# Optimization experiments

Hardware: AMD Instinct MI355X
Metric: run time of the kernel (lower is better)

Reference implementation:

```python
import jax, jax.numpy as jnp
import numpy as np

N_NODES = 100000
N_EDGES = 1600000
IN_F = 128
OUT_F = 32
HEADS = 4
NEG_SLOPE = 0.2
EPS = 1e-8


def setup_inputs() -> dict:
    key = jax.random.key(0)
    k1, k2, k3, k4 = jax.random.split(key, 4)
    x = jax.random.normal(k1, (N_NODES, IN_F), dtype=jnp.float32)
    # torch Linear weight layout: [out_features*num_heads, in_features]
    # xavier_uniform-like scale
    limW = float(np.sqrt(6.0 / (IN_F + OUT_F * HEADS)))
    W = jax.random.uniform(k2, (OUT_F * HEADS, IN_F), dtype=jnp.float32, minval=-limW, maxval=limW)
    lima = float(np.sqrt(6.0 / (HEADS + 2 * OUT_F)))
    a = jax.random.uniform(k3, (HEADS, 2 * OUT_F), dtype=jnp.float32, minval=-lima, maxval=lima)
    edge_index = jax.random.randint(k4, (2, N_EDGES), 0, N_NODES, dtype=jnp.int64)
    return {"x": x, "W": W, "a": a, "edge_index": edge_index}


def reference(x, W, a, edge_index):
    # x: [N, in], W: [H*F, in], a: [H, 2F], edge_index: [2, E]
    N = x.shape[0]
    H = HEADS
    F = OUT_F
    h = (x @ W.T).reshape(N, H, F)                      # [N, H, F]
    src, dst = edge_index[0], edge_index[1]
    h_src = h[src]                                       # [E, H, F]
    h_dst = h[dst]                                       # [E, H, F]
    # (cat([h_src, h_dst], -1) * a).sum(-1) == h_src@a_src + h_dst@a_dst
    a_src, a_dst = a[:, :F], a[:, F:]
    att = jnp.einsum('ehf,hf->eh', h_src, a_src) + jnp.einsum('ehf,hf->eh', h_dst, a_dst)  # [E, H]
    att = jnp.where(att >= 0, att, NEG_SLOPE * att)      # leaky_relu(0.2)
    att = jnp.exp(att - att.max())                       # global-max stabilization (as in source)
    att_sum = jax.ops.segment_sum(att, dst, num_segments=N)    # [N, H]
    att = att / (att_sum[dst] + EPS)                     # segment softmax
    # dropout is identity in eval mode
    out = jax.ops.segment_sum(att[..., None] * h_src, dst, num_segments=N)  # [N, H, F]
    return out.reshape(N, H * F)                         # concat=True
```

## Files before the change

kernel.cpp:

```cpp
#include <hip/hip_runtime.h>
#include <hip/hip_bf16.h>

#define NEG_SLOPE 0.2f
#define EPSV 1e-8f
#define BCAP 5632

typedef float f32x4 __attribute__((ext_vector_type(4)));
typedef short bf16x8 __attribute__((ext_vector_type(8)));
typedef unsigned short us8 __attribute__((ext_vector_type(8)));

static __device__ __forceinline__ float bf16tof(unsigned short s) {
    union { unsigned u; float f; } c; c.u = ((unsigned)s) << 16; return c.f;
}
static __device__ __forceinline__ unsigned short ftobf16(float f) {
    __hip_bfloat16 b = __float2bfloat16(f);
    return *(unsigned short*)&b;
}
static __device__ __forceinline__ float leaky_exp(float v) {
    v = fmaxf(v, NEG_SLOPE * v);
    return __expf(v);
}

__global__ __launch_bounds__(256, 2) void k_gemm_scatter(
        const float* __restrict__ x, const float* __restrict__ W,
        const float* __restrict__ a, unsigned short* __restrict__ h_bf,
        float* __restrict__ asrc, float* __restrict__ adst,
        const int* __restrict__ ei, int* __restrict__ relcur,
        unsigned* __restrict__ ebuf, int E, int N, int GB, int SB) {
    __shared__ unsigned short xs[128 * 128];
    __shared__ unsigned short ws[128 * 128];
    __shared__ float sa[256];
    int tid = threadIdx.x;
    int bid = blockIdx.x;

    int M = min(GB, SB);
    bool isGemm; int myIdx;
    if (bid < 2 * M) { isGemm = ((bid & 1) == 0); myIdx = bid >> 1; }
    else { isGemm = (GB > SB); myIdx = bid - M; }

    if (!isGemm) {
        int* hist  = (int*)xs;
        int* wcur  = hist + 512;
        int* bslot = wcur + 512;
        int lo = myIdx * 2048;
        int hi = min(E, lo + 2048);
        hist[tid] = 0; hist[tid + 256] = 0;
        wcur[tid] = 0; wcur[tid + 256] = 0;
        __syncthreads();
        int sreg[8], dreg[8];
#pragma unroll
        for (int k = 0; k < 8; k++) {
            int e = lo + tid + 256 * k;
            if (e < hi) {
                sreg[k] = ei[e];
                dreg[k] = ei[E + e];
                atomicAdd(&hist[dreg[k] >> 8], 1);
            }
        }
        __syncthreads();
        int c0 = hist[tid], c1 = hist[tid + 256];
        int r0 = c0 ? atomicAdd(&relcur[tid], c0) : 0;
        int r1 = c1 ? atomicAdd(&relcur[tid + 256], c1) : 0;
        bslot[tid]       = tid * BCAP + r0;
        bslot[tid + 256] = (tid + 256) * BCAP + r1;
        __syncthreads();
#pragma unroll
        for (int k = 0; k < 8; k++) {
            int e = lo + tid + 256 * k;
            if (e < hi) {
                int s = sreg[k];
                int d = dreg[k];
                int b = d >> 8;
                int off = atomicAdd(&wcur[b], 1);
                int slot = bslot[b] + off;
                if (slot < (b + 1) * BCAP)
                    ebuf[slot] = ((unsigned)(d & 255) << 23) | (unsigned)s;
            }
        }
        return;
    }

    int nb = myIdx * 128;
    sa[tid] = a[tid];

#pragma unroll
    for (int it = 0; it < 16; ++it) {
        int f = tid + 256 * it;
        int row = f >> 5;
        int k0 = (f & 31) << 2;
        int sw = row * 128 + (k0 ^ ((row & 7) << 3));
        int n = nb + row; if (n >= N) n = N - 1;
        float4 v = *(const float4*)(x + (size_t)n * 128 + k0);
        ushort4 o;
        o.x = ftobf16(v.x); o.y = ftobf16(v.y);
        o.z = ftobf16(v.z); o.w = ftobf16(v.w);
        *(ushort4*)&xs[sw] = o;
        float4 wv = *(const float4*)(W + (size_t)row * 128 + k0);
        ushort4 ow;
        ow.x = ftobf16(wv.x); ow.y = ftobf16(wv.y);
        ow.z = ftobf16(wv.z); ow.w = ftobf16(wv.w);
        *(ushort4*)&ws[sw] = ow;
    }
    __syncthreads();

    int w  = tid >> 6;
    int l  = tid & 63;
    int lr = l & 15;
    int lg = l >> 4;

    f32x4 acc[2][8];
    {
        f32x4 zz = {0.f, 0.f, 0.f, 0.f};
#pragma unroll
        for (int nt = 0; nt < 2; ++nt)
#pragma unroll
            for (int jt = 0; jt < 8; ++jt)
                acc[nt][jt] = zz;
    }

#pragma unroll
    for (int ks = 0; ks < 4; ++ks) {
        int kofs = ks * 32 + lg * 8;
        bf16x8 xf[2];
#pragma unroll
        for (int nt = 0; nt < 2; ++nt) {
            int row = w * 32 + nt * 16 + lr;
            xf[nt] = *(const bf16x8*)&xs[row * 128 + (kofs ^ ((row & 7) << 3))];
        }
#pragma unroll
        for (int jt = 0; jt < 8; ++jt) {
            int j = jt * 16 + lr;
            bf16x8 wf = *(const bf16x8*)&ws[j * 128 + (kofs ^ ((j & 7) << 3))];
#pragma unroll
            for (int nt = 0; nt < 2; ++nt)
                acc[nt][jt] = __builtin_amdgcn_mfma_f32_16x16x32_bf16(
                    wf, xf[nt], acc[nt][jt], 0, 0, 0);
        }
    }

#pragma unroll
    for (int g = 0; g < 4; ++g) {
        f32x4 as0 = *(const f32x4*)&sa[g * 64 +      lg * 4];
        f32x4 as1 = *(const f32x4*)&sa[g * 64 + 16 + lg * 4];
        f32x4 ad0 = *(const f32x4*)&sa[g * 64 + 32 + lg * 4];
        f32x4 ad1 = *(const f32x4*)&sa[g * 64 + 48 + lg * 4];
#pragma unroll
        for (int nt = 0; nt < 2; ++nt) {
            float ps = 0.f, pd = 0.f;
#pragma unroll
            for (int r = 0; r < 4; ++r) {
                ps += acc[nt][2 * g][r] * as0[r] + acc[nt][2 * g + 1][r] * as1[r];
                pd += acc[nt][2 * g][r] * ad0[r] + acc[nt][2 * g + 1][r] * ad1[r];
            }
            ps += __shfl_xor(ps, 16); pd += __shfl_xor(pd, 16);
            ps += __shfl_xor(ps, 32); pd += __shfl_xor(pd, 32);
            if (lg == 0) {
                int n = nb + w * 32 + nt * 16 + lr;
                if (n < N) {
                    asrc[(size_t)n * 4 + g] = ps;
                    adst[(size_t)n * 4 + g] = pd;
                }
            }
        }
    }

    __syncthreads();
#pragma unroll
    for (int nt = 0; nt < 2; ++nt) {
        int row = w * 32 + nt * 16 + lr;
        int m = (row & 7) << 3;
#pragma unroll
        for (int jt = 0; jt < 8; ++jt) {
            int j0 = jt * 16 + lg * 4;
            ushort4 o;
            o.x = ftobf16(acc[nt][jt][0]);
            o.y = ftobf16(acc[nt][jt][1]);
            o.z = ftobf16(acc[nt][jt][2]);
            o.w = ftobf16(acc[nt][jt][3]);
            *(ushort4*)&xs[row * 128 + (j0 ^ m)] = o;
        }
    }
    __syncthreads();
#pragma unroll
    for (int it = 0; it < 8; ++it) {
        int f = tid + 256 * it;
        int row = f >> 4;
        int c8 = (f & 15) << 3;
        int n = nb + row;
        if (n < N) {
            us8 v = *(const us8*)&xs[row * 128 + (c8 ^ ((row & 7) << 3))];
            *(us8*)(h_bf + (size_t)n * 128 + c8) = v;
        }
    }
}

__global__ __launch_bounds__(512) void k_build(const int* __restrict__ relcur,
        const unsigned* __restrict__ ebuf,
        int* __restrict__ row_ptr, int* __restrict__ csr_src,
        int NBK, int N, int E) {
    __shared__ int smA[512];
    __shared__ int hist[256];
    __shared__ int smB[256];
    int b = blockIdx.x;
    int t = threadIdx.x;

    smA[t] = (t < NBK) ? min(relcur[t], BCAP) : 0;
    __syncthreads();
    for (int off = 1; off < 512; off <<= 1) {
        int u = (t >= off) ? smA[t - off] : 0;
        __syncthreads();
        smA[t] += u;
        __syncthreads();
    }
    int cnt  = min(relcur[b], BCAP);
    int base = smA[b] - cnt;
    if (b == 0 && t == 0) row_ptr[N] = E;

    int d0 = b << 8;
    const unsigned* ep = ebuf + (size_t)b * BCAP;

    if (t < 256) hist[t] = 0;
    __syncthreads();
    unsigned pay[11]; int rnk[11];
#pragma unroll
    for (int k = 0; k < 11; ++k) {
        int i = t + 512 * k;
        if (i < cnt) {
            unsigned p = ep[i];
            pay[k] = p;
            rnk[k] = atomicAdd(&hist[p >> 23], 1);
        } else {
            pay[k] = 0u;
            rnk[k] = -1;
        }
    }
    __syncthreads();

    int s = (t < 256) ? hist[t] : 0;
    if (t < 256) smB[t] = s;
    __syncthreads();
    for (int off = 1; off < 256; off <<= 1) {
        int u = (t >= off && t < 256) ? smB[t - off] : 0;
        __syncthreads();
        if (t < 256) smB[t] += u;
        __syncthreads();
    }
    if (t < 256) {
        int ex = smB[t] - s;
        hist[t] = ex;
        int node = d0 + t;
        if (node < N) row_ptr[node] = base + ex;
    }
    __syncthreads();

#pragma unroll
    for (int k = 0; k < 11; ++k) {
        if (rnk[k] >= 0) {
            unsigned p = pay[k];
            csr_src[base + hist[p >> 23] + rnk[k]] = (int)(p & 0x7FFFFFu);
        }
    }
}

__global__ __launch_bounds__(256) void k_agg(
        const int* __restrict__ row_ptr, const int* __restrict__ csr_src,
        const float* __restrict__ asrc, const float* __restrict__ adst,
        const unsigned short* __restrict__ h_bf,
        float* __restrict__ out, int N) {
    __shared__ int   se[4][2][68];
    __shared__ float sw[4][2][272];
    int tid = threadIdx.x;
    int w  = tid >> 6;
    int l  = tid & 63;
    int gg = l >> 4;
    int m  = l & 15;
    int hh = m >> 2;

    int n = blockIdx.x * 16 + w * 4 + gg;
    bool valid = (n < N);
    int nc = valid ? n : (N - 1);
    int lo  = row_ptr[nc];
    int deg = row_ptr[nc + 1] - lo;
    float4 dv = *(const float4*)(adst + 4 * (size_t)nc);

    int md = deg;
    md = max(md, __shfl_xor(md, 16));
    md = max(md, __shfl_xor(md, 32));
    int nch = (md + 15) >> 4;

    float acc[8] = {};
    float asum = 0.f;
    const unsigned short* hp = h_bf + 8 * m;

#define ACC8(U, WT) do { \
        union { unsigned u; float f; } q; \
        q.u = (U).x << 16;         acc[0] += (WT) * q.f; \
        q.u = (U).x & 0xFFFF0000u; acc[1] += (WT) * q.f; \
        q.u = (U).y << 16;         acc[2] += (WT) * q.f; \
        q.u = (U).y & 0xFFFF0000u; acc[3] += (WT) * q.f; \
        q.u = (U).z << 16;         acc[4] += (WT) * q.f; \
        q.u = (U).z & 0xFFFF0000u; acc[5] += (WT) * q.f; \
        q.u = (U).w << 16;         acc[6] += (WT) * q.f; \
        q.u = (U).w & 0xFFFF0000u; acc[7] += (WT) * q.f; \
    } while (0)

    if (m < deg) {
        int s = csr_src[lo + m];
        se[w][0][17 * gg + m] = s;
        float4 sv = *(const float4*)(asrc + 4 * (size_t)s);
        float4 wv;
        wv.x = leaky_exp(sv.x + dv.x);
        wv.y = leaky_exp(sv.y + dv.y);
        wv.z = leaky_exp(sv.z + dv.z);
        wv.w = leaky_exp(sv.w + dv.w);
        *(float4*)&sw[w][0][68 * gg + 4 * m] = wv;
    }

    for (int c = 0; c < nch; ++c) {
        int cb = c & 1;
        int sN = 0; float4 svN; bool haveN = false;
        {
            int eN = (c + 1) * 16 + m;
            if (c + 1 < nch && eN < deg) {
                sN = csr_src[lo + eN];
                svN = *(const float4*)(asrc + 4 * (size_t)sN);
                haveN = true;
            }
        }
        __builtin_amdgcn_wave_barrier();
        int base16 = c * 16;
        int cnt = min(deg - base16, 16);
        const int*   sep = &se[w][cb][17 * gg];
        const float* swp = &sw[w][cb][68 * gg];
        int i = 0;
        uint4 u0, u1;
        if (cnt >= 2) {
            u0 = *(const uint4*)(hp + (size_t)sep[0] * 128);
            u1 = *(const uint4*)(hp + (size_t)sep[1] * 128);
        }
        for (; i + 4 <= cnt; i += 2) {
            uint4 t0 = *(const uint4*)(hp + (size_t)sep[i + 2] * 128);
            uint4 t1 = *(const uint4*)(hp + (size_t)sep[i + 3] * 128);
            float w0 = swp[4 * i + hh];
            float w1 = swp[4 * i + 4 + hh];
            ACC8(u0, w0);
            ACC8(u1, w1);
            asum += w0 + w1;
            u0 = t0; u1 = t1;
        }
        if (i + 2 <= cnt) {
            float w0 = swp[4 * i + hh];
            float w1 = swp[4 * i + 4 + hh];
            ACC8(u0, w0);
            ACC8(u1, w1);
            asum += w0 + w1;
            i += 2;
        }
        for (; i < cnt; ++i) {
            int s0 = sep[i];
            float w0 = swp[4 * i + hh];
            uint4 uu = *(const uint4*)(hp + (size_t)s0 * 128);
            ACC8(uu, w0);
            asum += w0;
        }
        if (haveN) {
            se[w][cb ^ 1][17 * gg + m] = sN;
            float4 wv;
            wv.x = leaky_exp(svN.x + dv.x);
            wv.y = leaky_exp(svN.y + dv.y);
            wv.z = leaky_exp(svN.z + dv.z);
            wv.w = leaky_exp(svN.w + dv.w);
            *(float4*)&sw[w][cb ^ 1][68 * gg + 4 * m] = wv;
        }
        __builtin_amdgcn_wave_barrier();
    }
#undef ACC8

    if (valid) {
        float inv = 1.f / (asum + EPSV);
        float4 o0, o1;
        o0.x = acc[0] * inv; o0.y = acc[1] * inv;
        o0.z = acc[2] * inv; o0.w = acc[3] * inv;
        o1.x = acc[4] * inv; o1.y = acc[5] * inv;
        o1.z = acc[6] * inv; o1.w = acc[7] * inv;
        *(float4*)(out + (size_t)n * 128 + 8 * m) = o0;
        *(float4*)(out + (size_t)n * 128 + 8 * m + 4) = o1;
    }
}

extern "C" void kernel_launch(void* const* d_in, const int* in_sizes, int n_in,
                              void* d_out, int out_size, void* d_ws, size_t ws_size,
                              hipStream_t stream) {
    const float* x = (const float*)d_in[0];
    const float* W = (const float*)d_in[1];
    const float* a = (const float*)d_in[2];
    const int* ei = (const int*)d_in[3];
    float* out = (float*)d_out;

    int N = in_sizes[0] / 128;
    int E = in_sizes[3] / 2;
    int NBK = (N + 255) >> 8;

    char* wsb = (char*)d_ws;
    size_t off = 0;
    auto alloc = [&](size_t bytes) -> void* {
        void* p = wsb + off;
        off += (bytes + 255) / 256 * 256;
        return p;
    };
    unsigned short* h_bf = (unsigned short*)alloc((size_t)N * 128 * 2);
    float* asrc = (float*)alloc((size_t)N * 4 * 4);
    float* adst = (float*)alloc((size_t)N * 4 * 4);
    int* row_ptr = (int*)alloc((size_t)(N + 1) * 4);
    int* relcur = (int*)alloc(512 * 4);
    unsigned* ebuf = (unsigned*)alloc((size_t)NBK * BCAP * 4);
    int* csr_src = (int*)alloc((size_t)E * 4);

    hipMemsetAsync(relcur, 0, 512 * 4, stream);

    int GB = (N + 127) / 128;
    int SB = (E + 2047) / 2048;
    k_gemm_scatter<<<GB + SB, 256, 0, stream>>>(x, W, a, h_bf, asrc, adst,
                                                ei, relcur, ebuf, E, N, GB, SB);
    k_build<<<NBK, 512, 0, stream>>>(relcur, ebuf, row_ptr, csr_src, NBK, N, E);
    k_agg<<<(N + 15) / 16, 256, 0, stream>>>(row_ptr, csr_src, asrc, adst, h_bf, out, N);
}
```

Baseline: 212.1 us.

## Fuse CSR build into aggregation kernel with per-bucket LDS adjacency

Merges the bucket-sort build kernel and the aggregation kernel into one kernel. Each block sorts its 128-destination bucket into an LDS CSR and then aggregates those nodes directly, which removes the global row_ptr/csr_src arrays, their write and re-read traffic, the global prefix scan, and one launch. Buckets shrink from 256 to 128 nodes with a smaller capacity, and scatter blocks each handle 4096 edges. The cost is fewer, larger aggregation blocks (782 blocks of 512 threads) with heavy LDS use, which may limit occupancy and load balance, and a tighter bucket capacity that could overflow on skewed graphs.

```diff
diff --git a/kernel.cpp b/kernel.cpp
--- a/kernel.cpp
+++ b/kernel.cpp
@@ -3,15 +3,12 @@
 
 #define NEG_SLOPE 0.2f
 #define EPSV 1e-8f
-#define BCAP 5632
+#define BCAP 3072
 
 typedef float f32x4 __attribute__((ext_vector_type(4)));
 typedef short bf16x8 __attribute__((ext_vector_type(8)));
 typedef unsigned short us8 __attribute__((ext_vector_type(8)));
 
-static __device__ __forceinline__ float bf16tof(unsigned short s) {
-    union { unsigned u; float f; } c; c.u = ((unsigned)s) << 16; return c.f;
-}
 static __device__ __forceinline__ unsigned short ftobf16(float f) {
     __hip_bfloat16 b = __float2bfloat16(f);
     return *(unsigned short*)&b;
@@ -40,41 +37,46 @@
 
     if (!isGemm) {
         int* hist  = (int*)xs;
-        int* wcur  = hist + 512;
-        int* bslot = wcur + 512;
-        int lo = myIdx * 2048;
-        int hi = min(E, lo + 2048);
-        hist[tid] = 0; hist[tid + 256] = 0;
-        wcur[tid] = 0; wcur[tid + 256] = 0;
+        int* wcur  = hist + 1024;
+        int* bslot = wcur + 1024;
+        int lo = myIdx * 4096;
+        int hi = min(E, lo + 4096);
+#pragma unroll
+        for (int j = 0; j < 4; ++j) {
+            hist[tid + 256 * j] = 0;
+            wcur[tid + 256 * j] = 0;
+        }
         __syncthreads();
-        int sreg[8], dreg[8];
-#pragma unroll
-        for (int k = 0; k < 8; k++) {
+        int sreg[16], dreg[16];
+#pragma unroll
+        for (int k = 0; k < 16; k++) {
             int e = lo + tid + 256 * k;
             if (e < hi) {
                 sreg[k] = ei[e];
                 dreg[k] = ei[E + e];
-                atomicAdd(&hist[dreg[k] >> 8], 1);
+                atomicAdd(&hist[dreg[k] >> 7], 1);
             }
         }
         __syncthreads();
-        int c0 = hist[tid], c1 = hist[tid + 256];
-        int r0 = c0 ? atomicAdd(&relcur[tid], c0) : 0;
-        int r1 = c1 ? atomicAdd(&relcur[tid + 256], c1) : 0;
-        bslot[tid]       = tid * BCAP + r0;
-        bslot[tid + 256] = (tid + 256) * BCAP + r1;
+#pragma unroll
+        for (int j = 0; j < 4; ++j) {
+            int bb = tid + 256 * j;
+            int c = hist[bb];
+            int r = c ? atomicAdd(&relcur[bb], c) : 0;
+            bslot[bb] = bb * BCAP + r;
+        }
         __syncthreads();
 #pragma unroll
-        for (int k = 0; k < 8; k++) {
+        for (int k = 0; k < 16; k++) {
             int e = lo + tid + 256 * k;
             if (e < hi) {
                 int s = sreg[k];
                 int d = dreg[k];
-                int b = d >> 8;
+                int b = d >> 7;
                 int off = atomicAdd(&wcur[b], 1);
                 int slot = bslot[b] + off;
                 if (slot < (b + 1) * BCAP)
-                    ebuf[slot] = ((unsigned)(d & 255) << 23) | (unsigned)s;
+                    ebuf[slot] = ((unsigned)(d & 127) << 23) | (unsigned)s;
             }
         }
         return;
@@ -194,36 +196,27 @@
     }
 }
 
-__global__ __launch_bounds__(512) void k_build(const int* __restrict__ relcur,
-        const unsigned* __restrict__ ebuf,
-        int* __restrict__ row_ptr, int* __restrict__ csr_src,
-        int NBK, int N, int E) {
-    __shared__ int smA[512];
-    __shared__ int hist[256];
-    __shared__ int smB[256];
+__global__ __launch_bounds__(512) void k_bagg(
+        const int* __restrict__ relcur, const unsigned* __restrict__ ebuf,
+        const float* __restrict__ asrc, const float* __restrict__ adst,
+        const unsigned short* __restrict__ h_bf,
+        float* __restrict__ out, int N) {
+    __shared__ int   csr_lds[BCAP];
+    __shared__ int   offx[128];
+    __shared__ int   dg[128];
+    __shared__ int   hist[128];
+    __shared__ int   smB[128];
+    __shared__ float swb[8][2][272];
     int b = blockIdx.x;
     int t = threadIdx.x;
-
-    smA[t] = (t < NBK) ? min(relcur[t], BCAP) : 0;
-    __syncthreads();
-    for (int off = 1; off < 512; off <<= 1) {
-        int u = (t >= off) ? smA[t - off] : 0;
-        __syncthreads();
-        smA[t] += u;
-        __syncthreads();
-    }
-    int cnt  = min(relcur[b], BCAP);
-    int base = smA[b] - cnt;
-    if (b == 0 && t == 0) row_ptr[N] = E;
-
-    int d0 = b << 8;
+    int cnt = min(relcur[b], BCAP);
     const unsigned* ep = ebuf + (size_t)b * BCAP;
 
-    if (t < 256) hist[t] = 0;
-    __syncthreads();
-    unsigned pay[11]; int rnk[11];
-#pragma unroll
-    for (int k = 0; k < 11; ++k) {
+    if (t < 128) hist[t] = 0;
+    __syncthreads();
+    unsigned pay[6]; int rnk[6];
+#pragma unroll
+    for (int k = 0; k < 6; ++k) {
         int i = t + 512 * k;
         if (i < cnt) {
             unsigned p = ep[i];
@@ -236,60 +229,31 @@
     }
     __syncthreads();
 
-    int s = (t < 256) ? hist[t] : 0;
-    if (t < 256) smB[t] = s;
-    __syncthreads();
-    for (int off = 1; off < 256; off <<= 1) {
-        int u = (t >= off && t < 256) ? smB[t - off] : 0;
+    if (t < 128) { int s = hist[t]; dg[t] = s; smB[t] = s; }
+    __syncthreads();
+    for (int off = 1; off < 128; off <<= 1) {
+        int u = (t >= off && t < 128) ? smB[t - off] : 0;
         __syncthreads();
-        if (t < 256) smB[t] += u;
+        if (t < 128) smB[t] += u;
         __syncthreads();
     }
-    if (t < 256) {
-        int ex = smB[t] - s;
-        hist[t] = ex;
-        int node = d0 + t;
-        if (node < N) row_ptr[node] = base + ex;
-    }
-    __syncthreads();
-
-#pragma unroll
-    for (int k = 0; k < 11; ++k) {
+    if (t < 128) offx[t] = smB[t] - dg[t];
+    __syncthreads();
+
+#pragma unroll
+    for (int k = 0; k < 6; ++k) {
         if (rnk[k] >= 0) {
             unsigned p = pay[k];
-            csr_src[base + hist[p >> 23] + rnk[k]] = (int)(p & 0x7FFFFFu);
-        }
-    }
-}
-
-__global__ __launch_bounds__(256) void k_agg(
-        const int* __restrict__ row_ptr, const int* __restrict__ csr_src,
-        const float* __restrict__ asrc, const float* __restrict__ adst,
-        const unsigned short* __restrict__ h_bf,
-        float* __restrict__ out, int N) {
-    __shared__ int   se[4][2][68];
-    __shared__ float sw[4][2][272];
-    int tid = threadIdx.x;
-    int w  = tid >> 6;
-    int l  = tid & 63;
+            csr_lds[offx[p >> 23] + rnk[k]] = (int)(p & 0x7FFFFFu);
+        }
+    }
+    __syncthreads();
+
+    int w  = t >> 6;
+    int l  = t & 63;
     int gg = l >> 4;
     int m  = l & 15;
     int hh = m >> 2;
-
-    int n = blockIdx.x * 16 + w * 4 + gg;
-    bool valid = (n < N);
-    int nc = valid ? n : (N - 1);
-    int lo  = row_ptr[nc];
-    int deg = row_ptr[nc + 1] - lo;
-    float4 dv = *(const float4*)(adst + 4 * (size_t)nc);
-
-    int md = deg;
-    md = max(md, __shfl_xor(md, 16));
-    md = max(md, __shfl_xor(md, 32));
-    int nch = (md + 15) >> 4;
-
-    float acc[8] = {};
-    float asum = 0.f;
     const unsigned short* hp = h_bf + 8 * m;
 
 #define ACC8(U, WT) do { \
@@ -304,88 +268,104 @@
         q.u = (U).w & 0xFFFF0000u; acc[7] += (WT) * q.f; \
     } while (0)
 
-    if (m < deg) {
-        int s = csr_src[lo + m];
-        se[w][0][17 * gg + m] = s;
-        float4 sv = *(const float4*)(asrc + 4 * (size_t)s);
-        float4 wv;
-        wv.x = leaky_exp(sv.x + dv.x);
-        wv.y = leaky_exp(sv.y + dv.y);
-        wv.z = leaky_exp(sv.z + dv.z);
-        wv.w = leaky_exp(sv.w + dv.w);
-        *(float4*)&sw[w][0][68 * gg + 4 * m] = wv;
-    }
-
-    for (int c = 0; c < nch; ++c) {
-        int cb = c & 1;
-        int sN = 0; float4 svN; bool haveN = false;
-        {
-            int eN = (c + 1) * 16 + m;
-            if (c + 1 < nch && eN < deg) {
-                sN = csr_src[lo + eN];
-                svN = *(const float4*)(asrc + 4 * (size_t)sN);
-                haveN = true;
-            }
+    for (int r = 0; r < 4; ++r) {
+        int nl = r * 32 + w * 4 + gg;
+        int n = (b << 7) + nl;
+        bool valid = (n < N);
+        int nc = valid ? n : (N - 1);
+        int lo  = offx[nl];
+        int deg = dg[nl];
+        float4 dv = *(const float4*)(adst + 4 * (size_t)nc);
+
+        int md = deg;
+        md = max(md, __shfl_xor(md, 16));
+        md = max(md, __shfl_xor(md, 32));
+        int nch = (md + 15) >> 4;
+
+        float acc[8] = {};
+        float asum = 0.f;
+
+        if (m < deg) {
+            int s = csr_lds[lo + m];
+            float4 sv = *(const float4*)(asrc + 4 * (size_t)s);
+            float4 wv;
+            wv.x = leaky_exp(sv.x + dv.x);
+            wv.y = leaky_exp(sv.y + dv.y);
+            wv.z = leaky_exp(sv.z + dv.z);
+            wv.w = leaky_exp(sv.w + dv.w);
+            *(float4*)&swb[w][0][68 * gg + 4 * m] = wv;
         }
         __builtin_amdgcn_wave_barrier();
-        int base16 = c * 16;
-        int cnt = min(deg - base16, 16);
-        const int*   sep = &se[w][cb][17 * gg];
-        const float* swp = &sw[w][cb][68 * gg];
-        int i = 0;
-        uint4 u0, u1;
-        if (cnt >= 2) {
-            u0 = *(const uint4*)(hp + (size_t)sep[0] * 128);
-            u1 = *(const uint4*)(hp + (size_t)sep[1] * 128);
-        }
-        for (; i + 4 <= cnt; i += 2) {
-            uint4 t0 = *(const uint4*)(hp + (size_t)sep[i + 2] * 128);
-            uint4 t1 = *(const uint4*)(hp + (size_t)sep[i + 3] * 128);
-            float w0 = swp[4 * i + hh];
-            float w1 = swp[4 * i + 4 + hh];
-            ACC8(u0, w0);
-            ACC8(u1, w1);
-            asum += w0 + w1;
-            u0 = t0; u1 = t1;
-        }
-        if (i + 2 <= cnt) {
-            float w0 = swp[4 * i + hh];
-            float w1 = swp[4 * i + 4 + hh];
-            ACC8(u0, w0);
-            ACC8(u1, w1);
-            asum += w0 + w1;
-            i += 2;
-        }
-        for (; i < cnt; ++i) {
-            int s0 = sep[i];
-            float w0 = swp[4 * i + hh];
-            uint4 uu = *(const uint4*)(hp + (size_t)s0 * 128);
-            ACC8(uu, w0);
-            asum += w0;
-        }
-        if (haveN) {
-            se[w][cb ^ 1][17 * gg + m] = sN;
-            float4 wv;
-            wv.x = leaky_exp(svN.x + dv.x);
-            wv.y = leaky_exp(svN.y + dv.y);
-            wv.z = leaky_exp(svN.z + dv.z);
-            wv.w = leaky_exp(svN.w + dv.w);
-            *(float4*)&sw[w][cb ^ 1][68 * gg + 4 * m] = wv;
-        }
-        __builtin_amdgcn_wave_barrier();
+
+        for (int c = 0; c < nch; ++c) {
+            int cb = c & 1;
+            int sN = 0; float4 svN; bool haveN = false;
+            {
+                int eN = (c + 1) * 16 + m;
+                if (c + 1 < nch && eN < deg) {
+                    sN = csr_lds[lo + eN];
+                    svN = *(const float4*)(asrc + 4 * (size_t)sN);
+                    haveN = true;
+                }
+            }
+            __builtin_amdgcn_wave_barrier();
+            int base16 = c * 16;
+            int ccnt = min(deg - base16, 16);
+            const int*   idp = &csr_lds[lo + base16];
+            const float* swp = &swb[w][cb][68 * gg];
+            int i = 0;
+            uint4 u0, u1;
+            if (ccnt >= 2) {
+                u0 = *(const uint4*)(hp + (size_t)idp[0] * 128);
+                u1 = *(const uint4*)(hp + (size_t)idp[1] * 128);
+            }
+            for (; i + 4 <= ccnt; i += 2) {
+                uint4 t0 = *(const uint4*)(hp + (size_t)idp[i + 2] * 128);
+                uint4 t1 = *(const uint4*)(hp + (size_t)idp[i + 3] * 128);
+                float w0 = swp[4 * i + hh];
+                float w1 = swp[4 * i + 4 + hh];
+                ACC8(u0, w0);
+                ACC8(u1, w1);
+                asum += w0 + w1;
+                u0 = t0; u1 = t1;
+            }
+            if (i + 2 <= ccnt) {
+                float w0 = swp[4 * i + hh];
+                float w1 = swp[4 * i + 4 + hh];
+                ACC8(u0, w0);
+                ACC8(u1, w1);
+                asum += w0 + w1;
+                i += 2;
+            }
+            for (; i < ccnt; ++i) {
+                float w0 = swp[4 * i + hh];
+                uint4 uu = *(const uint4*)(hp + (size_t)idp[i] * 128);
+                ACC8(uu, w0);
+                asum += w0;
+            }
+            if (haveN) {
+                float4 wv;
+                wv.x = leaky_exp(svN.x + dv.x);
+                wv.y = leaky_exp(svN.y + dv.y);
+                wv.z = leaky_exp(svN.z + dv.z);
+                wv.w = leaky_exp(svN.w + dv.w);
+                *(float4*)&swb[w][cb ^ 1][68 * gg + 4 * m] = wv;
+            }
+            __builtin_amdgcn_wave_barrier();
+        }
+
+        if (valid) {
+            float inv = 1.f / (asum + EPSV);
+            float4 o0, o1;
+            o0.x = acc[0] * inv; o0.y = acc[1] * inv;
+            o0.z = acc[2] * inv; o0.w = acc[3] * inv;
+            o1.x = acc[4] * inv; o1.y = acc[5] * inv;
+            o1.z = acc[6] * inv; o1.w = acc[7] * inv;
+            *(float4*)(out + (size_t)n * 128 + 8 * m) = o0;
+            *(float4*)(out + (size_t)n * 128 + 8 * m + 4) = o1;
+        }
     }
 #undef ACC8
-
-    if (valid) {
-        float inv = 1.f / (asum + EPSV);
-        float4 o0, o1;
-        o0.x = acc[0] * inv; o0.y = acc[1] * inv;
-        o0.z = acc[2] * inv; o0.w = acc[3] * inv;
-        o1.x = acc[4] * inv; o1.y = acc[5] * inv;
-        o1.z = acc[6] * inv; o1.w = acc[7] * inv;
-        *(float4*)(out + (size_t)n * 128 + 8 * m) = o0;
-        *(float4*)(out + (size_t)n * 128 + 8 * m + 4) = o1;
-    }
 }
 
 extern "C" void kernel_launch(void* const* d_in, const int* in_sizes, int n_in,
@@ -399,7 +379,7 @@
 
     int N = in_sizes[0] / 128;
     int E = in_sizes[3] / 2;
-    int NBK = (N + 255) >> 8;
+    int NBK = (N + 127) >> 7;
 
     char* wsb = (char*)d_ws;
     size_t off = 0;
@@ -411,17 +391,14 @@
     unsigned short* h_bf = (unsigned short*)alloc((size_t)N * 128 * 2);
     float* asrc = (float*)alloc((size_t)N * 4 * 4);
     float* adst = (float*)alloc((size_t)N * 4 * 4);
-    int* row_ptr = (int*)alloc((size_t)(N + 1) * 4);
-    int* relcur = (int*)alloc(512 * 4);
+    int* relcur = (int*)alloc(1024 * 4);
     unsigned* ebuf = (unsigned*)alloc((size_t)NBK * BCAP * 4);
-    int* csr_src = (int*)alloc((size_t)E * 4);
-
-    hipMemsetAsync(relcur, 0, 512 * 4, stream);
+
+    hipMemsetAsync(relcur, 0, 1024 * 4, stream);
 
     int GB = (N + 127) / 128;
-    int SB = (E + 2047) / 2048;
+    int SB = (E + 4095) / 4096;
     k_gemm_scatter<<<GB + SB, 256, 0, stream>>>(x, W, a, h_bf, asrc, adst,
                                                 ei, relcur, ebuf, E, N, GB, SB);
-    k_build<<<NBK, 512, 0, stream>>>(relcur, ebuf, row_ptr, csr_src, NBK, N, E);
-    k_agg<<<(N + 15) / 16, 256, 0, stream>>>(row_ptr, csr_src, asrc, adst, h_bf, out, N);
+    k_bagg<<<NBK, 512, 0, stream>>>(relcur, ebuf, asrc, adst, h_bf, out, N);
 }
```

Result: slower. 224.1 us (+5.6%).

## Split aggregation into two feature-half passes with 8 lanes per node

Applied to the files above, without the earlier changes.

The aggregation kernel now runs twice, each pass covering half of the 128 features (two heads), with 8 lanes per node instead of 16 so that 32 nodes are handled per block. Each pass gathers only 128 bytes of h per source row, which shrinks the gather working set per pass and may improve cache hit rates. In exchange, row_ptr, csr_src and the attention scores are read twice, the exp weights are computed twice, and there is an extra kernel launch.

```diff
diff --git a/kernel.cpp b/kernel.cpp
--- a/kernel.cpp
+++ b/kernel.cpp
@@ -9,9 +9,6 @@
 typedef short bf16x8 __attribute__((ext_vector_type(8)));
 typedef unsigned short us8 __attribute__((ext_vector_type(8)));
 
-static __device__ __forceinline__ float bf16tof(unsigned short s) {
-    union { unsigned u; float f; } c; c.u = ((unsigned)s) << 16; return c.f;
-}
 static __device__ __forceinline__ unsigned short ftobf16(float f) {
     __hip_bfloat16 b = __float2bfloat16(f);
     return *(unsigned short*)&b;
@@ -266,31 +263,32 @@
         const int* __restrict__ row_ptr, const int* __restrict__ csr_src,
         const float* __restrict__ asrc, const float* __restrict__ adst,
         const unsigned short* __restrict__ h_bf,
-        float* __restrict__ out, int N) {
-    __shared__ int   se[4][2][68];
-    __shared__ float sw[4][2][272];
+        float* __restrict__ out, int N, int fh) {
+    __shared__ int   se[4][2][8 * 17];
+    __shared__ float sw[4][2][8 * 34];
     int tid = threadIdx.x;
     int w  = tid >> 6;
     int l  = tid & 63;
-    int gg = l >> 4;
-    int m  = l & 15;
+    int gg = l >> 3;
+    int m  = l & 7;
     int hh = m >> 2;
 
-    int n = blockIdx.x * 16 + w * 4 + gg;
+    int n = blockIdx.x * 32 + w * 8 + gg;
     bool valid = (n < N);
     int nc = valid ? n : (N - 1);
     int lo  = row_ptr[nc];
     int deg = row_ptr[nc + 1] - lo;
-    float4 dv = *(const float4*)(adst + 4 * (size_t)nc);
+    float2 dv = *(const float2*)(adst + 4 * (size_t)nc + 2 * fh);
 
     int md = deg;
+    md = max(md, __shfl_xor(md, 8));
     md = max(md, __shfl_xor(md, 16));
     md = max(md, __shfl_xor(md, 32));
     int nch = (md + 15) >> 4;
 
     float acc[8] = {};
     float asum = 0.f;
-    const unsigned short* hp = h_bf + 8 * m;
+    const unsigned short* hp = h_bf + 64 * fh + 8 * m;
 
 #define ACC8(U, WT) do { \
         union { unsigned u; float f; } q; \
@@ -304,34 +302,47 @@
         q.u = (U).w & 0xFFFF0000u; acc[7] += (WT) * q.f; \
     } while (0)
 
-    if (m < deg) {
-        int s = csr_src[lo + m];
-        se[w][0][17 * gg + m] = s;
-        float4 sv = *(const float4*)(asrc + 4 * (size_t)s);
-        float4 wv;
-        wv.x = leaky_exp(sv.x + dv.x);
-        wv.y = leaky_exp(sv.y + dv.y);
-        wv.z = leaky_exp(sv.z + dv.z);
-        wv.w = leaky_exp(sv.w + dv.w);
-        *(float4*)&sw[w][0][68 * gg + 4 * m] = wv;
+    {
+#pragma unroll
+        for (int half = 0; half < 2; ++half) {
+            int e = m + 8 * half;
+            if (e < deg) {
+                int s = csr_src[lo + e];
+                se[w][0][17 * gg + e] = s;
+                float2 sv = *(const float2*)(asrc + 4 * (size_t)s + 2 * fh);
+                float2 wv;
+                wv.x = leaky_exp(sv.x + dv.x);
+                wv.y = leaky_exp(sv.y + dv.y);
+                *(float2*)&sw[w][0][34 * gg + 2 * e] = wv;
+            }
+        }
     }
 
     for (int c = 0; c < nch; ++c) {
         int cb = c & 1;
-        int sN = 0; float4 svN; bool haveN = false;
+        int sN1 = 0, sN2 = 0; float2 svN1, svN2;
+        bool haveN1 = false, haveN2 = false;
         {
-            int eN = (c + 1) * 16 + m;
-            if (c + 1 < nch && eN < deg) {
-                sN = csr_src[lo + eN];
-                svN = *(const float4*)(asrc + 4 * (size_t)sN);
-                haveN = true;
+            int eb = (c + 1) * 16;
+            if (c + 1 < nch) {
+                int e1 = eb + m, e2 = eb + m + 8;
+                if (e1 < deg) {
+                    sN1 = csr_src[lo + e1];
+                    svN1 = *(const float2*)(asrc + 4 * (size_t)sN1 + 2 * fh);
+                    haveN1 = true;
+                }
+                if (e2 < deg) {
+                    sN2 = csr_src[lo + e2];
+                    svN2 = *(const float2*)(asrc + 4 * (size_t)sN2 + 2 * fh);
+                    haveN2 = true;
+                }
             }
         }
         __builtin_amdgcn_wave_barrier();
         int base16 = c * 16;
         int cnt = min(deg - base16, 16);
         const int*   sep = &se[w][cb][17 * gg];
-        const float* swp = &sw[w][cb][68 * gg];
+        const float* swp = &sw[w][cb][34 * gg];
         int i = 0;
         uint4 u0, u1;
         if (cnt >= 2) {
@@ -341,16 +352,16 @@
         for (; i + 4 <= cnt; i += 2) {
             uint4 t0 = *(const uint4*)(hp + (size_t)sep[i + 2] * 128);
             uint4 t1 = *(const uint4*)(hp + (size_t)sep[i + 3] * 128);
-            float w0 = swp[4 * i + hh];
-            float w1 = swp[4 * i + 4 + hh];
+            float w0 = swp[2 * i + hh];
+            float w1 = swp[2 * i + 2 + hh];
             ACC8(u0, w0);
             ACC8(u1, w1);
             asum += w0 + w1;
             u0 = t0; u1 = t1;
         }
         if (i + 2 <= cnt) {
-            float w0 = swp[4 * i + hh];
-            float w1 = swp[4 * i + 4 + hh];
+            float w0 = swp[2 * i + hh];
+            float w1 = swp[2 * i + 2 + hh];
             ACC8(u0, w0);
             ACC8(u1, w1);
             asum += w0 + w1;
@@ -358,19 +369,24 @@
         }
         for (; i < cnt; ++i) {
             int s0 = sep[i];
-            float w0 = swp[4 * i + hh];
+            float w0 = swp[2 * i + hh];
             uint4 uu = *(const uint4*)(hp + (size_t)s0 * 128);
             ACC8(uu, w0);
             asum += w0;
         }
-        if (haveN) {
-            se[w][cb ^ 1][17 * gg + m] = sN;
-            float4 wv;
-            wv.x = leaky_exp(svN.x + dv.x);
-            wv.y = leaky_exp(svN.y + dv.y);
-            wv.z = leaky_exp(svN.z + dv.z);
-            wv.w = leaky_exp(svN.w + dv.w);
-            *(float4*)&sw[w][cb ^ 1][68 * gg + 4 * m] = wv;
+        if (haveN1) {
+            se[w][cb ^ 1][17 * gg + m] = sN1;
+            float2 wv;
+            wv.x = leaky_exp(svN1.x + dv.x);
+            wv.y = leaky_exp(svN1.y + dv.y);
+            *(float2*)&sw[w][cb ^ 1][34 * gg + 2 * m] = wv;
+        }
+        if (haveN2) {
+            se[w][cb ^ 1][17 * gg + m + 8] = sN2;
+            float2 wv;
+            wv.x = leaky_exp(svN2.x + dv.x);
+            wv.y = leaky_exp(svN2.y + dv.y);
+            *(float2*)&sw[w][cb ^ 1][34 * gg + 2 * m + 16] = wv;
         }
         __builtin_amdgcn_wave_barrier();
     }
@@ -383,8 +399,9 @@
         o0.z = acc[2] * inv; o0.w = acc[3] * inv;
         o1.x = acc[4] * inv; o1.y = acc[5] * inv;
         o1.z = acc[6] * inv; o1.w = acc[7] * inv;
-        *(float4*)(out + (size_t)n * 128 + 8 * m) = o0;
-        *(float4*)(out + (size_t)n * 128 + 8 * m + 4) = o1;
+        float* op = out + (size_t)n * 128 + 64 * fh + 8 * m;
+        *(float4*)op = o0;
+        *(float4*)(op + 4) = o1;
     }
 }
 
@@ -423,5 +440,7 @@
     k_gemm_scatter<<<GB + SB, 256, 0, stream>>>(x, W, a, h_bf, asrc, adst,
                                                 ei, relcur, ebuf, E, N, GB, SB);
     k_build<<<NBK, 512, 0, stream>>>(relcur, ebuf, row_ptr, csr_src, NBK, N, E);
-    k_agg<<<(N + 15) / 16, 256, 0, stream>>>(row_ptr, csr_src, asrc, adst, h_bf, out, N);
-}
+    int AGB = (N + 31) / 32;
+    k_agg<<<AGB, 256, 0, stream>>>(row_ptr, csr_src, asrc, adst, h_bf, out, N, 0);
+    k_agg<<<AGB, 256, 0, stream>>>(row_ptr, csr_src, asrc, adst, h_bf, out, N, 1);
+}
```

Measured after the change: 220.3 us. +3.9%, slower.

## Fuse CSR build and aggregation into one cooperative persistent kernel

Applied to the files above, without the earlier changes.

Merges the CSR build and aggregation kernels into one cooperative kernel, separated by a grid-wide sync. Both phases become grid-stride loops, which removes one kernel launch boundary. The build phase now ranks edges by scanning the bucket twice with shared atomics instead of holding payloads in registers. Aggregation uses 512-thread blocks covering 32 nodes per iteration. This adds a grid sync and nondeterministic CSR ordering, and occupancy is limited by the fixed persistent grid size.

```diff
diff --git a/kernel.cpp b/kernel.cpp
--- a/kernel.cpp
+++ b/kernel.cpp
@@ -1,17 +1,17 @@
 #include <hip/hip_runtime.h>
 #include <hip/hip_bf16.h>
+#include <hip/hip_cooperative_groups.h>
 
 #define NEG_SLOPE 0.2f
 #define EPSV 1e-8f
 #define BCAP 5632
 
+namespace cg = cooperative_groups;
+
 typedef float f32x4 __attribute__((ext_vector_type(4)));
 typedef short bf16x8 __attribute__((ext_vector_type(8)));
 typedef unsigned short us8 __attribute__((ext_vector_type(8)));
 
-static __device__ __forceinline__ float bf16tof(unsigned short s) {
-    union { unsigned u; float f; } c; c.u = ((unsigned)s) << 16; return c.f;
-}
 static __device__ __forceinline__ unsigned short ftobf16(float f) {
     __hip_bfloat16 b = __float2bfloat16(f);
     return *(unsigned short*)&b;
@@ -194,102 +194,75 @@
     }
 }
 
-__global__ __launch_bounds__(512) void k_build(const int* __restrict__ relcur,
-        const unsigned* __restrict__ ebuf,
+__global__ __launch_bounds__(512, 6) void k_coop(
+        const int* __restrict__ relcur, const unsigned* __restrict__ ebuf,
+        const float* __restrict__ asrc, const float* __restrict__ adst,
+        const unsigned short* __restrict__ h_bf, float* __restrict__ out,
         int* __restrict__ row_ptr, int* __restrict__ csr_src,
         int NBK, int N, int E) {
+    cg::grid_group grid = cg::this_grid();
     __shared__ int smA[512];
     __shared__ int hist[256];
     __shared__ int smB[256];
+    __shared__ int excl[256];
+    __shared__ int   se[8][2][68];
+    __shared__ float swb[8][2][272];
     int b = blockIdx.x;
     int t = threadIdx.x;
-
-    smA[t] = (t < NBK) ? min(relcur[t], BCAP) : 0;
-    __syncthreads();
-    for (int off = 1; off < 512; off <<= 1) {
-        int u = (t >= off) ? smA[t - off] : 0;
-        __syncthreads();
-        smA[t] += u;
-        __syncthreads();
-    }
-    int cnt  = min(relcur[b], BCAP);
-    int base = smA[b] - cnt;
+    int G = gridDim.x;
+
     if (b == 0 && t == 0) row_ptr[N] = E;
-
-    int d0 = b << 8;
-    const unsigned* ep = ebuf + (size_t)b * BCAP;
-
-    if (t < 256) hist[t] = 0;
-    __syncthreads();
-    unsigned pay[11]; int rnk[11];
-#pragma unroll
-    for (int k = 0; k < 11; ++k) {
-        int i = t + 512 * k;
-        if (i < cnt) {
+    for (int q = b; q < NBK; q += G) {
+        smA[t] = (t < NBK) ? min(relcur[t], BCAP) : 0;
+        __syncthreads();
+        for (int off = 1; off < 512; off <<= 1) {
+            int u = (t >= off) ? smA[t - off] : 0;
+            __syncthreads();
+            smA[t] += u;
+            __syncthreads();
+        }
+        int cnt  = min(relcur[q], BCAP);
+        int base = smA[q] - cnt;
+        int d0 = q << 8;
+        const unsigned* ep = ebuf + (size_t)q * BCAP;
+
+        if (t < 256) hist[t] = 0;
+        __syncthreads();
+        for (int i = t; i < cnt; i += 512)
+            atomicAdd(&hist[ep[i] >> 23], 1);
+        __syncthreads();
+
+        int s = (t < 256) ? hist[t] : 0;
+        if (t < 256) smB[t] = s;
+        __syncthreads();
+        for (int off = 1; off < 256; off <<= 1) {
+            int u = (t >= off && t < 256) ? smB[t - off] : 0;
+            __syncthreads();
+            if (t < 256) smB[t] += u;
+            __syncthreads();
+        }
+        if (t < 256) {
+            int ex = smB[t] - s;
+            excl[t] = ex;
+            int node = d0 + t;
+            if (node < N) row_ptr[node] = base + ex;
+        }
+        __syncthreads();
+
+        for (int i = t; i < cnt; i += 512) {
             unsigned p = ep[i];
-            pay[k] = p;
-            rnk[k] = atomicAdd(&hist[p >> 23], 1);
-        } else {
-            pay[k] = 0u;
-            rnk[k] = -1;
-        }
-    }
-    __syncthreads();
-
-    int s = (t < 256) ? hist[t] : 0;
-    if (t < 256) smB[t] = s;
-    __syncthreads();
-    for (int off = 1; off < 256; off <<= 1) {
-        int u = (t >= off && t < 256) ? smB[t - off] : 0;
-        __syncthreads();
-        if (t < 256) smB[t] += u;
-        __syncthreads();
-    }
-    if (t < 256) {
-        int ex = smB[t] - s;
-        hist[t] = ex;
-        int node = d0 + t;
-        if (node < N) row_ptr[node] = base + ex;
-    }
-    __syncthreads();
-
-#pragma unroll
-    for (int k = 0; k < 11; ++k) {
-        if (rnk[k] >= 0) {
-            unsigned p = pay[k];
-            csr_src[base + hist[p >> 23] + rnk[k]] = (int)(p & 0x7FFFFFu);
-        }
-    }
-}
-
-__global__ __launch_bounds__(256) void k_agg(
-        const int* __restrict__ row_ptr, const int* __restrict__ csr_src,
-        const float* __restrict__ asrc, const float* __restrict__ adst,
-        const unsigned short* __restrict__ h_bf,
-        float* __restrict__ out, int N) {
-    __shared__ int   se[4][2][68];
-    __shared__ float sw[4][2][272];
-    int tid = threadIdx.x;
-    int w  = tid >> 6;
-    int l  = tid & 63;
-    int gg = l >> 4;
+            int pos = base + atomicAdd(&excl[p >> 23], 1);
+            csr_src[pos] = (int)(p & 0x7FFFFFu);
+        }
+        __syncthreads();
+    }
+    grid.sync();
+
+    int w  = t >> 6;
+    int l  = t & 63;
+    int sg = l >> 4;
     int m  = l & 15;
     int hh = m >> 2;
-
-    int n = blockIdx.x * 16 + w * 4 + gg;
-    bool valid = (n < N);
-    int nc = valid ? n : (N - 1);
-    int lo  = row_ptr[nc];
-    int deg = row_ptr[nc + 1] - lo;
-    float4 dv = *(const float4*)(adst + 4 * (size_t)nc);
-
-    int md = deg;
-    md = max(md, __shfl_xor(md, 16));
-    md = max(md, __shfl_xor(md, 32));
-    int nch = (md + 15) >> 4;
-
-    float acc[8] = {};
-    float asum = 0.f;
     const unsigned short* hp = h_bf + 8 * m;
 
 #define ACC8(U, WT) do { \
@@ -304,88 +277,107 @@
         q.u = (U).w & 0xFFFF0000u; acc[7] += (WT) * q.f; \
     } while (0)
 
-    if (m < deg) {
-        int s = csr_src[lo + m];
-        se[w][0][17 * gg + m] = s;
-        float4 sv = *(const float4*)(asrc + 4 * (size_t)s);
-        float4 wv;
-        wv.x = leaky_exp(sv.x + dv.x);
-        wv.y = leaky_exp(sv.y + dv.y);
-        wv.z = leaky_exp(sv.z + dv.z);
-        wv.w = leaky_exp(sv.w + dv.w);
-        *(float4*)&sw[w][0][68 * gg + 4 * m] = wv;
-    }
-
-    for (int c = 0; c < nch; ++c) {
-        int cb = c & 1;
-        int sN = 0; float4 svN; bool haveN = false;
-        {
-            int eN = (c + 1) * 16 + m;
-            if (c + 1 < nch && eN < deg) {
-                sN = csr_src[lo + eN];
-                svN = *(const float4*)(asrc + 4 * (size_t)sN);
-                haveN = true;
-            }
+    int NG = (N + 31) >> 5;
+    for (int grp = b; grp < NG; grp += G) {
+        int n = grp * 32 + w * 4 + sg;
+        bool valid = (n < N);
+        int nc = valid ? n : (N - 1);
+        int lo  = row_ptr[nc];
+        int deg = row_ptr[nc + 1] - lo;
+        float4 dv = *(const float4*)(adst + 4 * (size_t)nc);
+
+        int md = deg;
+        md = max(md, __shfl_xor(md, 16));
+        md = max(md, __shfl_xor(md, 32));
+        int nch = (md + 15) >> 4;
+
+        float acc[8] = {};
+        float asum = 0.f;
+
+        if (m < deg) {
+            int s = csr_src[lo + m];
+            se[w][0][17 * sg + m] = s;
+            float4 sv = *(const float4*)(asrc + 4 * (size_t)s);
+            float4 wv;
+            wv.x = leaky_exp(sv.x + dv.x);
+            wv.y = leaky_exp(sv.y + dv.y);
+            wv.z = leaky_exp(sv.z + dv.z);
+            wv.w = leaky_exp(sv.w + dv.w);
+            *(float4*)&swb[w][0][68 * sg + 4 * m] = wv;
         }
         __builtin_amdgcn_wave_barrier();
-        int base16 = c * 16;
-        int cnt = min(deg - base16, 16);
-        const int*   sep = &se[w][cb][17 * gg];
-        const float* swp = &sw[w][cb][68 * gg];
-        int i = 0;
-        uint4 u0, u1;
-        if (cnt >= 2) {
-            u0 = *(const uint4*)(hp + (size_t)sep[0] * 128);
-            u1 = *(const uint4*)(hp + (size_t)sep[1] * 128);
-        }
-        for (; i + 4 <= cnt; i += 2) {
-            uint4 t0 = *(const uint4*)(hp + (size_t)sep[i + 2] * 128);
-            uint4 t1 = *(const uint4*)(hp + (size_t)sep[i + 3] * 128);
-            float w0 = swp[4 * i + hh];
-            float w1 = swp[4 * i + 4 + hh];
-            ACC8(u0, w0);
-            ACC8(u1, w1);
-            asum += w0 + w1;
-            u0 = t0; u1 = t1;
-        }
-        if (i + 2 <= cnt) {
-            float w0 = swp[4 * i + hh];
-            float w1 = swp[4 * i + 4 + hh];
-            ACC8(u0, w0);
-            ACC8(u1, w1);
-            asum += w0 + w1;
-            i += 2;
-        }
-        for (; i < cnt; ++i) {
-            int s0 = sep[i];
-            float w0 = swp[4 * i + hh];
-            uint4 uu = *(const uint4*)(hp + (size_t)s0 * 128);
-            ACC8(uu, w0);
-            asum += w0;
-        }
-        if (haveN) {
-            se[w][cb ^ 1][17 * gg + m] = sN;
-            float4 wv;
-            wv.x = leaky_exp(svN.x + dv.x);
-            wv.y = leaky_exp(svN.y + dv.y);
-            wv.z = leaky_exp(svN.z + dv.z);
-            wv.w = leaky_exp(svN.w + dv.w);
-            *(float4*)&sw[w][cb ^ 1][68 * gg + 4 * m] = wv;
-        }
-        __builtin_amdgcn_wave_barrier();
+
+        for (int c = 0; c < nch; ++c) {
+            int cb = c & 1;
+            int sN = 0; float4 svN; bool haveN = false;
+            {
+                int eN = (c + 1) * 16 + m;
+                if (c + 1 < nch && eN < deg) {
+                    sN = csr_src[lo + eN];
+                    svN = *(const float4*)(asrc + 4 * (size_t)sN);
+                    haveN = true;
+                }
+            }
+            __builtin_amdgcn_wave_barrier();
+            int base16 = c * 16;
+            int cnt = min(deg - base16, 16);
+            const int*   sep = &se[w][cb][17 * sg];
+            const float* swp = &swb[w][cb][68 * sg];
+            int i = 0;
+            uint4 u0, u1;
+            if (cnt >= 2) {
+                u0 = *(const uint4*)(hp + (size_t)sep[0] * 128);
+                u1 = *(const uint4*)(hp + (size_t)sep[1] * 128);
+            }
+            for (; i + 4 <= cnt; i += 2) {
+                uint4 t0 = *(const uint4*)(hp + (size_t)sep[i + 2] * 128);
+                uint4 t1 = *(const uint4*)(hp + (size_t)sep[i + 3] * 128);
+                float w0 = swp[4 * i + hh];
+                float w1 = swp[4 * i + 4 + hh];
+                ACC8(u0, w0);
+                ACC8(u1, w1);
+                asum += w0 + w1;
+                u0 = t0; u1 = t1;
+            }
+            if (i + 2 <= cnt) {
+                float w0 = swp[4 * i + hh];
+                float w1 = swp[4 * i + 4 + hh];
+                ACC8(u0, w0);
+                ACC8(u1, w1);
+                asum += w0 + w1;
+                i += 2;
+            }
+            for (; i < cnt; ++i) {
+                int s0 = sep[i];
+                float w0 = swp[4 * i + hh];
+                uint4 uu = *(const uint4*)(hp + (size_t)s0 * 128);
+                ACC8(uu, w0);
+                asum += w0;
+            }
+            if (haveN) {
+                se[w][cb ^ 1][17 * sg + m] = sN;
+                float4 wv;
+                wv.x = leaky_exp(svN.x + dv.x);
+                wv.y = leaky_exp(svN.y + dv.y);
+                wv.z = leaky_exp(svN.z + dv.z);
+                wv.w = leaky_exp(svN.w + dv.w);
+                *(float4*)&swb[w][cb ^ 1][68 * sg + 4 * m] = wv;
+            }
+            __builtin_amdgcn_wave_barrier();
+        }
+
+        if (valid) {
+            float inv = 1.f / (asum + EPSV);
+            float4 o0, o1;
+            o0.x = acc[0] * inv; o0.y = acc[1] * inv;
+            o0.z = acc[2] * inv; o0.w = acc[3] * inv;
+            o1.x = acc[4] * inv; o1.y = acc[5] * inv;
+            o1.z = acc[6] * inv; o1.w = acc[7] * inv;
+            *(float4*)(out + (size_t)n * 128 + 8 * m) = o0;
+            *(float4*)(out + (size_t)n * 128 + 8 * m + 4) = o1;
+        }
     }
 #undef ACC8
-
-    if (valid) {
-        float inv = 1.f / (asum + EPSV);
-        float4 o0, o1;
-        o0.x = acc[0] * inv; o0.y = acc[1] * inv;
-        o0.z = acc[2] * inv; o0.w = acc[3] * inv;
-        o1.x = acc[4] * inv; o1.y = acc[5] * inv;
-        o1.z = acc[6] * inv; o1.w = acc[7] * inv;
-        *(float4*)(out + (size_t)n * 128 + 8 * m) = o0;
-        *(float4*)(out + (size_t)n * 128 + 8 * m + 4) = o1;
-    }
 }
 
 extern "C" void kernel_launch(void* const* d_in, const int* in_sizes, int n_in,
@@ -422,6 +414,17 @@
     int SB = (E + 2047) / 2048;
     k_gemm_scatter<<<GB + SB, 256, 0, stream>>>(x, W, a, h_bf, asrc, adst,
                                                 ei, relcur, ebuf, E, N, GB, SB);
-    k_build<<<NBK, 512, 0, stream>>>(relcur, ebuf, row_ptr, csr_src, NBK, N, E);
-    k_agg<<<(N + 15) / 16, 256, 0, stream>>>(row_ptr, csr_src, asrc, adst, h_bf, out, N);
+
+    int maxB = 0;
+    if (hipOccupancyMaxActiveBlocksPerMultiprocessor(&maxB, (const void*)k_coop,
+                                                     512, 0) != hipSuccess || maxB < 1)
+        maxB = 2;
+    int G = maxB * 256;
+    if (G > 2048) G = 2048;
+
+    void* kargs[] = { (void*)&relcur, (void*)&ebuf, (void*)&asrc, (void*)&adst,
+                      (void*)&h_bf, (void*)&out, (void*)&row_ptr, (void*)&csr_src,
+                      (void*)&NBK, (void*)&N, (void*)&E };
+    hipLaunchCooperativeKernel((const void*)k_coop, dim3(G), dim3(512),
+                               kargs, 0, stream);
 }
```

Result: slower. 300.4 us (+41.6%).
